# Optimization experiments

Measured on AMD Instinct MI355X. Metric: run time of the kernel, lower is better.

The kernel has to match this reference:

```python
import jax, jax.numpy as jnp
import numpy as np

N_TRIALS, T, INPUT_DIM = 32, 512, 64
N, R, OUTPUT_DIM = 4096, 8, 64
DT = 0.1


def setup_inputs() -> dict:
    key = jax.random.key(0)
    k_inp, k_B, k_W, k_m, k_n = jax.random.split(key, 5)
    inp = jax.random.normal(k_inp, (N_TRIALS, T, INPUT_DIM), dtype=jnp.float32)
    B = jax.random.normal(k_B, (N, INPUT_DIM), dtype=jnp.float32)
    W = jax.random.normal(k_W, (OUTPUT_DIM, N), dtype=jnp.float32) / np.sqrt(N)
    m = jax.random.normal(k_m, (N, R), dtype=jnp.float32)
    n = jax.random.normal(k_n, (N, R), dtype=jnp.float32)
    return {"inp": inp, "B": B, "W": W, "m": m, "n": n}


def reference(inp, B, W, m, n):
    # inp: [b, t, i]; B: [N, i]; W: [o, N]; m, n: [N, r]
    n_trials = inp.shape[0]
    # Precompute input projection for all steps: [t, b, N]
    inp_proj = jnp.einsum('bti,ni->tbn', inp, B)

    def step(x, u):
        # x: [b, N] voltage; u: [b, N] projected input at this step
        # sigmoid(x) @ (m n^T / N)^T == ((sigmoid(x) @ n) @ m^T) / N
        rec = (jax.nn.sigmoid(x) @ n) @ m.T / N
        x_new = (1.0 - DT) * x + DT * (rec + u)
        y = jax.nn.sigmoid(x_new) @ W.T  # [b, o]
        return x_new, (x_new, y)

    x0 = jnp.zeros((n_trials, N), dtype=inp.dtype)
    _, (xs, ys) = jax.lax.scan(step, x0, inp_proj)
    # xs: [t, b, N]; ys: [t, b, o]
    x_seq = jnp.concatenate([x0[None], xs], axis=0).transpose(1, 0, 2)  # [b, t+1, N]
    output_seq = ys.transpose(1, 0, 2)  # [b, t, o]
    return (x_seq, output_seq)
```

## Files before the change

### kernel.cpp

```cpp
#include <hip/hip_runtime.h>

static constexpr int BTRIALS = 32;
static constexpr int TSTEPS  = 512;
static constexpr int IDIM    = 64;
static constexpr int NDIM    = 4096;
static constexpr int RDIM    = 8;
static constexpr int ODIM    = 64;

typedef short v8s __attribute__((ext_vector_type(8)));
typedef float v4f __attribute__((ext_vector_type(4)));

__device__ __forceinline__ float fast_sigmoid(float x) {
    float e = __builtin_amdgcn_exp2f(x * -1.44269504088896340736f);
    return __builtin_amdgcn_rcpf(1.0f + e);
}

__device__ __forceinline__ float2 pk_fma(float2 a, float2 b, float2 c) {
    float2 d;
    asm("v_pk_fma_f32 %0, %1, %2, %3" : "=v"(d) : "v"(a), "v"(b), "v"(c));
    return d;
}

template <int CTRL, int RMASK>
__device__ __forceinline__ float dpp_add(float v) {
    int moved = __builtin_amdgcn_update_dpp(0, __float_as_int(v), CTRL, RMASK, 0xf, true);
    return v + __int_as_float(moved);
}

__device__ __forceinline__ float wave_reduce_to_lane63(float v) {
    v = dpp_add<0x111, 0xf>(v);
    v = dpp_add<0x112, 0xf>(v);
    v = dpp_add<0x114, 0xf>(v);
    v = dpp_add<0x118, 0xf>(v);
    v = dpp_add<0x142, 0xa>(v);
    v = dpp_add<0x143, 0xc>(v);
    return v;
}

__device__ __forceinline__ short f2bf(float f) {
    unsigned u = __float_as_uint(f);
    u += 0x7FFFu + ((u >> 16) & 1u);
    return (short)(u >> 16);
}

__global__ __launch_bounds__(256) void split_conv(const float* __restrict__ src,
                                                  unsigned short* __restrict__ hi,
                                                  unsigned short* __restrict__ lo,
                                                  float scale) {
    const int base = (blockIdx.x * 256 + threadIdx.x) * 8;
    float4 a = *(const float4*)(src + base);
    float4 b = *(const float4*)(src + base + 4);
    float v[8] = {a.x, a.y, a.z, a.w, b.x, b.y, b.z, b.w};
    v8s h, l;
    #pragma unroll
    for (int j = 0; j < 8; ++j) {
        float f  = v[j] * scale;
        short hb = f2bf(f);
        h[j] = hb;
        float fh = __uint_as_float(((unsigned)(unsigned short)hb) << 16);
        l[j] = f2bf(f - fh);
    }
    *(v8s*)(hi + base) = h;
    *(v8s*)(lo + base) = l;
}

__global__ __launch_bounds__(256) void wconv(const float* __restrict__ W,
                                             unsigned short* __restrict__ Wb) {
    const int base = (blockIdx.x * 256 + threadIdx.x) * 8;
    float4 a = *(const float4*)(W + base);
    float4 b = *(const float4*)(W + base + 4);
    v8s o;
    o[0] = f2bf(a.x); o[1] = f2bf(a.y); o[2] = f2bf(a.z); o[3] = f2bf(a.w);
    o[4] = f2bf(b.x); o[5] = f2bf(b.y); o[6] = f2bf(b.z); o[7] = f2bf(b.w);
    *(v8s*)(Wb + base) = o;
}

__global__ __launch_bounds__(256) void pre_gemm_mfma(const unsigned short* __restrict__ Ah,
                                                     const unsigned short* __restrict__ Al,
                                                     const unsigned short* __restrict__ Bh,
                                                     const unsigned short* __restrict__ Bl,
                                                     float* __restrict__ u, int t0) {
    const int tid  = threadIdx.x;
    const int lane = tid & 63;
    const int wv   = tid >> 6;
    const int lm   = lane & 15;
    const int kq   = lane >> 4;

    const int mloc = blockIdx.x * 16 + lm;
    const int b    = mloc & 31;
    const int t    = t0 + (mloc >> 5);
    const size_t arow = (size_t)b * TSTEPS + t;

    const unsigned short* pah = Ah + arow * IDIM + kq * 8;
    const unsigned short* pal = Al + arow * IDIM + kq * 8;
    v8s ah0 = *(const v8s*)(pah);
    v8s ah1 = *(const v8s*)(pah + 32);
    v8s al0 = *(const v8s*)(pal);
    v8s al1 = *(const v8s*)(pal + 32);

    const int n0   = wv * 1024;
    const int urow = blockIdx.x * 16 + kq * 4;

    #pragma unroll 2
    for (int nt = 0; nt < 64; ++nt) {
        const int n = n0 + nt * 16 + lm;
        const unsigned short* pbh = Bh + (size_t)n * IDIM + kq * 8;
        const unsigned short* pbl = Bl + (size_t)n * IDIM + kq * 8;
        v8s bh0 = *(const v8s*)(pbh);
        v8s bh1 = *(const v8s*)(pbh + 32);
        v8s bl0 = *(const v8s*)(pbl);
        v8s bl1 = *(const v8s*)(pbl + 32);
        v4f acc = (v4f){0.f, 0.f, 0.f, 0.f};
        acc = __builtin_amdgcn_mfma_f32_16x16x32_bf16(ah0, bl0, acc, 0, 0, 0);
        acc = __builtin_amdgcn_mfma_f32_16x16x32_bf16(al0, bh0, acc, 0, 0, 0);
        acc = __builtin_amdgcn_mfma_f32_16x16x32_bf16(ah1, bl1, acc, 0, 0, 0);
        acc = __builtin_amdgcn_mfma_f32_16x16x32_bf16(al1, bh1, acc, 0, 0, 0);
        acc = __builtin_amdgcn_mfma_f32_16x16x32_bf16(ah0, bh0, acc, 0, 0, 0);
        acc = __builtin_amdgcn_mfma_f32_16x16x32_bf16(ah1, bh1, acc, 0, 0, 0);
        float* up = u + (size_t)urow * NDIM + n0 + nt * 16 + lm;
        #pragma unroll
        for (int r = 0; r < 4; ++r) up[(size_t)r * NDIM] = acc[r];
    }
}

__global__ __launch_bounds__(512, 2) void scan_kernel(const float* __restrict__ mmat,
                                                      const float* __restrict__ nmat,
                                                      const float* __restrict__ u,
                                                      float* __restrict__ xseq,
                                                      float* __restrict__ xstate,
                                                      unsigned short* __restrict__ sbuf,
                                                      int t0, int tc) {
    const int b    = blockIdx.x;
    const int tid  = threadIdx.x;
    const int j0   = tid * 8;
    const int lane = tid & 63;
    const int wv   = tid >> 6;

    __shared__ __align__(16) float wlds[2][64];

    float2 nmp[4][8], mmp[4][8], x2[4], sp[4];
    const float mscale = 0.1f / 4096.0f;
    #pragma unroll
    for (int jp = 0; jp < 4; ++jp) {
        const float4* na = (const float4*)(nmat + (size_t)(j0 + 2 * jp) * RDIM);
        float4 a0 = na[0], a1 = na[1], b0 = na[2], b1 = na[3];
        nmp[jp][0] = {a0.x, b0.x}; nmp[jp][1] = {a0.y, b0.y};
        nmp[jp][2] = {a0.z, b0.z}; nmp[jp][3] = {a0.w, b0.w};
        nmp[jp][4] = {a1.x, b1.x}; nmp[jp][5] = {a1.y, b1.y};
        nmp[jp][6] = {a1.z, b1.z}; nmp[jp][7] = {a1.w, b1.w};
        const float4* ma = (const float4*)(mmat + (size_t)(j0 + 2 * jp) * RDIM);
        float4 d0 = ma[0], d1 = ma[1], e0 = ma[2], e1 = ma[3];
        mmp[jp][0] = {d0.x * mscale, e0.x * mscale}; mmp[jp][1] = {d0.y * mscale, e0.y * mscale};
        mmp[jp][2] = {d0.z * mscale, e0.z * mscale}; mmp[jp][3] = {d0.w * mscale, e0.w * mscale};
        mmp[jp][4] = {d1.x * mscale, e1.x * mscale}; mmp[jp][5] = {d1.y * mscale, e1.y * mscale};
        mmp[jp][6] = {d1.z * mscale, e1.z * mscale}; mmp[jp][7] = {d1.w * mscale, e1.w * mscale};
    }

    if (t0 == 0) {
        #pragma unroll
        for (int jp = 0; jp < 4; ++jp) x2[jp] = {0.f, 0.f};
        float* z = xseq + (size_t)b * (TSTEPS + 1) * NDIM + j0;
        *(float4*)(z + 0) = make_float4(0.f, 0.f, 0.f, 0.f);
        *(float4*)(z + 4) = make_float4(0.f, 0.f, 0.f, 0.f);
    } else {
        const float* xs = xstate + (size_t)b * NDIM + j0;
        float4 v0 = *(const float4*)(xs + 0);
        float4 v1 = *(const float4*)(xs + 4);
        x2[0] = {v0.x, v0.y}; x2[1] = {v0.z, v0.w};
        x2[2] = {v1.x, v1.y}; x2[3] = {v1.z, v1.w};
    }
    #pragma unroll
    for (int jp = 0; jp < 4; ++jp)
        sp[jp] = {fast_sigmoid(x2[jp].x), fast_sigmoid(x2[jp].y)};

    float2 uvp[4];
    {
        const float* up = u + ((size_t)0 * BTRIALS + b) * NDIM + j0;
        float4 v0 = *(const float4*)(up + 0);
        float4 v1 = *(const float4*)(up + 4);
        uvp[0] = {v0.x, v0.y}; uvp[1] = {v0.z, v0.w};
        uvp[2] = {v1.x, v1.y}; uvp[3] = {v1.z, v1.w};
    }
    const float2 c09 = {0.9f, 0.9f};

    for (int tl = 0; tl < tc; ++tl) {
        const int buf = tl & 1;
        const int tn = (tl + 1 < tc) ? (tl + 1) : tl;
        const float* upn = u + ((size_t)tn * BTRIALS + b) * NDIM + j0;
        float4 pf0 = *(const float4*)(upn + 0);
        float4 pf1 = *(const float4*)(upn + 4);

        float2 p2[8];
        #pragma unroll
        for (int r = 0; r < 8; ++r) p2[r] = {0.f, 0.f};
        #pragma unroll
        for (int jp = 0; jp < 4; ++jp) {
            #pragma unroll
            for (int r = 0; r < 8; ++r) p2[r] = pk_fma(sp[jp], nmp[jp][r], p2[r]);
        }
        float part[8];
        #pragma unroll
        for (int r = 0; r < 8; ++r) part[r] = p2[r].x + p2[r].y;
        #pragma unroll
        for (int r = 0; r < 8; ++r) part[r] = wave_reduce_to_lane63(part[r]);

        if (lane == 63) {
            #pragma unroll
            for (int r = 0; r < 8; ++r) wlds[buf][r * 8 + wv] = part[r];
        }

        float2 xd2[4];
        #pragma unroll
        for (int jp = 0; jp < 4; ++jp) xd2[jp] = pk_fma(c09, x2[jp], uvp[jp]);

        __syncthreads();

        float v = wlds[buf][lane];
        v = dpp_add<0x111, 0xf>(v);
        v = dpp_add<0x112, 0xf>(v);
        v = dpp_add<0x114, 0xf>(v);

        float ps[8];
        #pragma unroll
        for (int r = 0; r < 8; ++r)
            ps[r] = __int_as_float(__builtin_amdgcn_readlane(__float_as_int(v), r * 8 + 7));

        #pragma unroll
        for (int r = 0; r < 8; ++r) {
            float2 psr = {ps[r], ps[r]};
            #pragma unroll
            for (int jp = 0; jp < 4; ++jp) xd2[jp] = pk_fma(psr, mmp[jp][r], xd2[jp]);
        }
        #pragma unroll
        for (int jp = 0; jp < 4; ++jp) x2[jp] = xd2[jp];

        float* xrow = xseq + ((size_t)b * (TSTEPS + 1) + (t0 + tl + 1)) * NDIM + j0;
        *(float4*)(xrow + 0) = make_float4(x2[0].x, x2[0].y, x2[1].x, x2[1].y);
        *(float4*)(xrow + 4) = make_float4(x2[2].x, x2[2].y, x2[3].x, x2[3].y);

        #pragma unroll
        for (int jp = 0; jp < 4; ++jp)
            sp[jp] = {fast_sigmoid(x2[jp].x), fast_sigmoid(x2[jp].y)};
        int c0, c1, c2, c3;
        asm("v_cvt_pk_bf16_f32 %0, %1, %2" : "=v"(c0) : "v"(sp[0].x), "v"(sp[0].y));
        asm("v_cvt_pk_bf16_f32 %0, %1, %2" : "=v"(c1) : "v"(sp[1].x), "v"(sp[1].y));
        asm("v_cvt_pk_bf16_f32 %0, %1, %2" : "=v"(c2) : "v"(sp[2].x), "v"(sp[2].y));
        asm("v_cvt_pk_bf16_f32 %0, %1, %2" : "=v"(c3) : "v"(sp[3].x), "v"(sp[3].y));
        *(int4*)((void*)(sbuf + ((size_t)b * tc + tl) * NDIM + j0)) = make_int4(c0, c1, c2, c3);

        uvp[0] = {pf0.x, pf0.y}; uvp[1] = {pf0.z, pf0.w};
        uvp[2] = {pf1.x, pf1.y}; uvp[3] = {pf1.z, pf1.w};
    }

    float* xs = xstate + (size_t)b * NDIM + j0;
    *(float4*)(xs + 0) = make_float4(x2[0].x, x2[0].y, x2[1].x, x2[1].y);
    *(float4*)(xs + 4) = make_float4(x2[2].x, x2[2].y, x2[3].x, x2[3].y);
}

__global__ __launch_bounds__(256) void y_gemm(const unsigned short* __restrict__ sbuf,
                                              const unsigned short* __restrict__ Wb,
                                              float* __restrict__ yout,
                                              int t0, int tc) {
    const int tid  = threadIdx.x;
    const int lane = tid & 63;
    const int w    = blockIdx.x * 4 + (tid >> 6);
    const int mt   = w >> 1;
    const int ob   = (w & 1) << 1;
    const int lm   = lane & 15;
    const int kq   = lane >> 4;

    const int tilesPerB = tc >> 4;
    const int b  = mt / tilesPerB;
    const int tt = mt % tilesPerB;

    const unsigned short* pa = sbuf + ((size_t)b * tc + tt * 16 + lm) * NDIM + kq * 8;
    const unsigned short* pw0 = Wb + (size_t)(ob * 16 + lm) * NDIM + kq * 8;
    const unsigned short* pw1 = pw0 + (size_t)16 * NDIM;

    v4f acc0 = (v4f){0.f, 0.f, 0.f, 0.f};
    v4f acc1 = (v4f){0.f, 0.f, 0.f, 0.f};

    #pragma unroll 4
    for (int kc = 0; kc < NDIM; kc += 32) {
        v8s af = *(const v8s*)(pa + kc);
        v8s bf0 = *(const v8s*)(pw0 + kc);
        v8s bf1 = *(const v8s*)(pw1 + kc);
        acc0 = __builtin_amdgcn_mfma_f32_16x16x32_bf16(af, bf0, acc0, 0, 0, 0);
        acc1 = __builtin_amdgcn_mfma_f32_16x16x32_bf16(af, bf1, acc1, 0, 0, 0);
    }

    #pragma unroll
    for (int r = 0; r < 4; ++r) {
        const int row = b * TSTEPS + t0 + tt * 16 + kq * 4 + r;
        yout[(size_t)row * ODIM + (ob + 0) * 16 + lm] = acc0[r];
        yout[(size_t)row * ODIM + (ob + 1) * 16 + lm] = acc1[r];
    }
}

extern "C" void kernel_launch(void* const* d_in, const int* in_sizes, int n_in,
                              void* d_out, int out_size, void* d_ws, size_t ws_size,
                              hipStream_t stream) {
    const float* inp = (const float*)d_in[0];
    const float* Bm  = (const float*)d_in[1];
    const float* Wm  = (const float*)d_in[2];
    const float* mm  = (const float*)d_in[3];
    const float* nm  = (const float*)d_in[4];

    float* out  = (float*)d_out;
    float* xseq = out;
    float* yout = out + (size_t)BTRIALS * (TSTEPS + 1) * NDIM;

    float* xstate      = (float*)d_ws;
    unsigned short* Wb = (unsigned short*)(xstate + (size_t)BTRIALS * NDIM);
    unsigned short* Ah = Wb + (size_t)ODIM * NDIM;
    unsigned short* Al = Ah + (size_t)BTRIALS * TSTEPS * IDIM;
    unsigned short* Bh = Al + (size_t)BTRIALS * TSTEPS * IDIM;
    unsigned short* Bl = Bh + (size_t)NDIM * IDIM;
    float* ubuf        = (float*)(Bl + (size_t)NDIM * IDIM);

    const size_t head = (size_t)((char*)ubuf - (char*)d_ws);
    const size_t perstep = (size_t)BTRIALS * NDIM * (sizeof(float) + sizeof(unsigned short));
    size_t avail = (ws_size > head) ? (ws_size - head) : 0;
    int Tc = (int)(avail / perstep);
    if (Tc > TSTEPS) Tc = TSTEPS;
    Tc &= ~15;
    if (Tc < 16) Tc = 16;

    wconv<<<(ODIM * NDIM) / (256 * 8), 256, 0, stream>>>(Wm, Wb);
    split_conv<<<(BTRIALS * TSTEPS * IDIM) / (256 * 8), 256, 0, stream>>>(inp, Ah, Al, 0.1f);
    split_conv<<<(NDIM * IDIM) / (256 * 8), 256, 0, stream>>>(Bm, Bh, Bl, 1.0f);

    for (int t0 = 0; t0 < TSTEPS; t0 += Tc) {
        const int tc = (TSTEPS - t0 < Tc) ? (TSTEPS - t0) : Tc;
        unsigned short* sbuf = (unsigned short*)(ubuf + (size_t)tc * BTRIALS * NDIM);
        const int rows = tc * BTRIALS;
        pre_gemm_mfma<<<rows / 16, 256, 0, stream>>>(Ah, Al, Bh, Bl, ubuf, t0);
        scan_kernel<<<BTRIALS, 512, 0, stream>>>(mm, nm, ubuf, xseq, xstate, sbuf, t0, tc);
        const int mtiles = BTRIALS * (tc / 16);
        y_gemm<<<mtiles / 2, 256, 0, stream>>>(sbuf, Wb, yout, t0, tc);
    }
}
```

Measured before the change: 1.071 ms.

## Fuse pre-GEMM, scan and output GEMM into one persistent flag-synchronised kernel

Replaces the per-chunk sequence of three kernel launches with a single persistent kernel. 32 blocks run the recurrent scan, one per trial, while the remaining 224 blocks act as workers that compute the input projection and the output GEMM. Workers signal chunk completion through atomic flags in workspace, so the scan can start on a chunk as soon as its input projection is ready and the y GEMM can run behind the scan, overlapping the three stages. The scheme depends on all 256 blocks being co-resident and on spin-waits with a timeout break. It also requires a workspace large enough to hold u and sbuf for all 512 timesteps, and the flags share the start of the workspace with the former x-state region.

```diff
diff --git a/kernel.cpp b/kernel.cpp
--- a/kernel.cpp
+++ b/kernel.cpp
@@ -6,6 +6,17 @@
 static constexpr int NDIM    = 4096;
 static constexpr int RDIM    = 8;
 static constexpr int ODIM    = 64;
+
+static constexpr int TC   = 64;
+static constexpr int NCH  = TSTEPS / TC;
+static constexpr int SCAN_BLOCKS  = 32;
+static constexpr int TOTAL_BLOCKS = 256;
+static constexpr int WORKER_WAVES = (TOTAL_BLOCKS - SCAN_BLOCKS) * 8;
+static constexpr int PRE_TASKS_PER_CHUNK = 512;
+static constexpr int PRE_TASKS = NCH * PRE_TASKS_PER_CHUNK;
+static constexpr int Y_TASKS_PER_CHUNK = 256;
+static constexpr int Y_TASKS = NCH * Y_TASKS_PER_CHUNK;
+
 
 typedef short v8s __attribute__((ext_vector_type(8)));
 typedef float v4f __attribute__((ext_vector_type(4)));
@@ -65,7 +76,11 @@
 }
 
 __global__ __launch_bounds__(256) void wconv(const float* __restrict__ W,
-                                             unsigned short* __restrict__ Wb) {
+                                             unsigned short* __restrict__ Wb,
+                                             unsigned* __restrict__ flags) {
+    if (blockIdx.x == 0) {
+        for (int i = threadIdx.x; i < 1024; i += 256) flags[i] = 0;
+    }
     const int base = (blockIdx.x * 256 + threadIdx.x) * 8;
     float4 a = *(const float4*)(W + base);
     float4 b = *(const float4*)(W + base + 4);
@@ -75,225 +90,250 @@
     *(v8s*)(Wb + base) = o;
 }
 
-__global__ __launch_bounds__(256) void pre_gemm_mfma(const unsigned short* __restrict__ Ah,
-                                                     const unsigned short* __restrict__ Al,
-                                                     const unsigned short* __restrict__ Bh,
-                                                     const unsigned short* __restrict__ Bl,
-                                                     float* __restrict__ u, int t0) {
+__global__ __launch_bounds__(512) void mega(const unsigned short* __restrict__ Ah,
+                                            const unsigned short* __restrict__ Al,
+                                            const unsigned short* __restrict__ Bh,
+                                            const unsigned short* __restrict__ Bl,
+                                            const float* __restrict__ mmat,
+                                            const float* __restrict__ nmat,
+                                            float* __restrict__ u,
+                                            float* __restrict__ xseq,
+                                            unsigned short* __restrict__ sbuf,
+                                            const unsigned short* __restrict__ Wb,
+                                            float* __restrict__ yout,
+                                            unsigned* __restrict__ flags) {
+    __shared__ __align__(16) float wlds[2][64];
     const int tid  = threadIdx.x;
     const int lane = tid & 63;
-    const int wv   = tid >> 6;
-    const int lm   = lane & 15;
-    const int kq   = lane >> 4;
-
-    const int mloc = blockIdx.x * 16 + lm;
-    const int b    = mloc & 31;
-    const int t    = t0 + (mloc >> 5);
-    const size_t arow = (size_t)b * TSTEPS + t;
-
-    const unsigned short* pah = Ah + arow * IDIM + kq * 8;
-    const unsigned short* pal = Al + arow * IDIM + kq * 8;
-    v8s ah0 = *(const v8s*)(pah);
-    v8s ah1 = *(const v8s*)(pah + 32);
-    v8s al0 = *(const v8s*)(pal);
-    v8s al1 = *(const v8s*)(pal + 32);
-
-    const int n0   = wv * 1024;
-    const int urow = blockIdx.x * 16 + kq * 4;
-
-    #pragma unroll 2
-    for (int nt = 0; nt < 64; ++nt) {
-        const int n = n0 + nt * 16 + lm;
-        const unsigned short* pbh = Bh + (size_t)n * IDIM + kq * 8;
-        const unsigned short* pbl = Bl + (size_t)n * IDIM + kq * 8;
-        v8s bh0 = *(const v8s*)(pbh);
-        v8s bh1 = *(const v8s*)(pbh + 32);
-        v8s bl0 = *(const v8s*)(pbl);
-        v8s bl1 = *(const v8s*)(pbl + 32);
-        v4f acc = (v4f){0.f, 0.f, 0.f, 0.f};
-        acc = __builtin_amdgcn_mfma_f32_16x16x32_bf16(ah0, bl0, acc, 0, 0, 0);
-        acc = __builtin_amdgcn_mfma_f32_16x16x32_bf16(al0, bh0, acc, 0, 0, 0);
-        acc = __builtin_amdgcn_mfma_f32_16x16x32_bf16(ah1, bl1, acc, 0, 0, 0);
-        acc = __builtin_amdgcn_mfma_f32_16x16x32_bf16(al1, bh1, acc, 0, 0, 0);
-        acc = __builtin_amdgcn_mfma_f32_16x16x32_bf16(ah0, bh0, acc, 0, 0, 0);
-        acc = __builtin_amdgcn_mfma_f32_16x16x32_bf16(ah1, bh1, acc, 0, 0, 0);
-        float* up = u + (size_t)urow * NDIM + n0 + nt * 16 + lm;
+
+    if (blockIdx.x < SCAN_BLOCKS) {
+        const int b  = blockIdx.x;
+        const int j0 = tid * 8;
+        const int wv = tid >> 6;
+
+        float2 nmp[4][8], mmp[4][8], x2[4], sp[4];
+        const float mscale = 0.1f / 4096.0f;
         #pragma unroll
-        for (int r = 0; r < 4; ++r) up[(size_t)r * NDIM] = acc[r];
-    }
-}
-
-__global__ __launch_bounds__(512, 2) void scan_kernel(const float* __restrict__ mmat,
-                                                      const float* __restrict__ nmat,
-                                                      const float* __restrict__ u,
-                                                      float* __restrict__ xseq,
-                                                      float* __restrict__ xstate,
-                                                      unsigned short* __restrict__ sbuf,
-                                                      int t0, int tc) {
-    const int b    = blockIdx.x;
-    const int tid  = threadIdx.x;
-    const int j0   = tid * 8;
-    const int lane = tid & 63;
-    const int wv   = tid >> 6;
-
-    __shared__ __align__(16) float wlds[2][64];
-
-    float2 nmp[4][8], mmp[4][8], x2[4], sp[4];
-    const float mscale = 0.1f / 4096.0f;
-    #pragma unroll
-    for (int jp = 0; jp < 4; ++jp) {
-        const float4* na = (const float4*)(nmat + (size_t)(j0 + 2 * jp) * RDIM);
-        float4 a0 = na[0], a1 = na[1], b0 = na[2], b1 = na[3];
-        nmp[jp][0] = {a0.x, b0.x}; nmp[jp][1] = {a0.y, b0.y};
-        nmp[jp][2] = {a0.z, b0.z}; nmp[jp][3] = {a0.w, b0.w};
-        nmp[jp][4] = {a1.x, b1.x}; nmp[jp][5] = {a1.y, b1.y};
-        nmp[jp][6] = {a1.z, b1.z}; nmp[jp][7] = {a1.w, b1.w};
-        const float4* ma = (const float4*)(mmat + (size_t)(j0 + 2 * jp) * RDIM);
-        float4 d0 = ma[0], d1 = ma[1], e0 = ma[2], e1 = ma[3];
-        mmp[jp][0] = {d0.x * mscale, e0.x * mscale}; mmp[jp][1] = {d0.y * mscale, e0.y * mscale};
-        mmp[jp][2] = {d0.z * mscale, e0.z * mscale}; mmp[jp][3] = {d0.w * mscale, e0.w * mscale};
-        mmp[jp][4] = {d1.x * mscale, e1.x * mscale}; mmp[jp][5] = {d1.y * mscale, e1.y * mscale};
-        mmp[jp][6] = {d1.z * mscale, e1.z * mscale}; mmp[jp][7] = {d1.w * mscale, e1.w * mscale};
-    }
-
-    if (t0 == 0) {
+        for (int jp = 0; jp < 4; ++jp) {
+            const float4* na = (const float4*)(nmat + (size_t)(j0 + 2 * jp) * RDIM);
+            float4 a0 = na[0], a1 = na[1], b0 = na[2], b1 = na[3];
+            nmp[jp][0] = {a0.x, b0.x}; nmp[jp][1] = {a0.y, b0.y};
+            nmp[jp][2] = {a0.z, b0.z}; nmp[jp][3] = {a0.w, b0.w};
+            nmp[jp][4] = {a1.x, b1.x}; nmp[jp][5] = {a1.y, b1.y};
+            nmp[jp][6] = {a1.z, b1.z}; nmp[jp][7] = {a1.w, b1.w};
+            const float4* ma = (const float4*)(mmat + (size_t)(j0 + 2 * jp) * RDIM);
+            float4 d0 = ma[0], d1 = ma[1], e0 = ma[2], e1 = ma[3];
+            mmp[jp][0] = {d0.x * mscale, e0.x * mscale}; mmp[jp][1] = {d0.y * mscale, e0.y * mscale};
+            mmp[jp][2] = {d0.z * mscale, e0.z * mscale}; mmp[jp][3] = {d0.w * mscale, e0.w * mscale};
+            mmp[jp][4] = {d1.x * mscale, e1.x * mscale}; mmp[jp][5] = {d1.y * mscale, e1.y * mscale};
+            mmp[jp][6] = {d1.z * mscale, e1.z * mscale}; mmp[jp][7] = {d1.w * mscale, e1.w * mscale};
+        }
+
         #pragma unroll
         for (int jp = 0; jp < 4; ++jp) x2[jp] = {0.f, 0.f};
-        float* z = xseq + (size_t)b * (TSTEPS + 1) * NDIM + j0;
-        *(float4*)(z + 0) = make_float4(0.f, 0.f, 0.f, 0.f);
-        *(float4*)(z + 4) = make_float4(0.f, 0.f, 0.f, 0.f);
-    } else {
-        const float* xs = xstate + (size_t)b * NDIM + j0;
-        float4 v0 = *(const float4*)(xs + 0);
-        float4 v1 = *(const float4*)(xs + 4);
-        x2[0] = {v0.x, v0.y}; x2[1] = {v0.z, v0.w};
-        x2[2] = {v1.x, v1.y}; x2[3] = {v1.z, v1.w};
-    }
-    #pragma unroll
-    for (int jp = 0; jp < 4; ++jp)
-        sp[jp] = {fast_sigmoid(x2[jp].x), fast_sigmoid(x2[jp].y)};
-
-    float2 uvp[4];
-    {
-        const float* up = u + ((size_t)0 * BTRIALS + b) * NDIM + j0;
-        float4 v0 = *(const float4*)(up + 0);
-        float4 v1 = *(const float4*)(up + 4);
-        uvp[0] = {v0.x, v0.y}; uvp[1] = {v0.z, v0.w};
-        uvp[2] = {v1.x, v1.y}; uvp[3] = {v1.z, v1.w};
-    }
-    const float2 c09 = {0.9f, 0.9f};
-
-    for (int tl = 0; tl < tc; ++tl) {
-        const int buf = tl & 1;
-        const int tn = (tl + 1 < tc) ? (tl + 1) : tl;
-        const float* upn = u + ((size_t)tn * BTRIALS + b) * NDIM + j0;
-        float4 pf0 = *(const float4*)(upn + 0);
-        float4 pf1 = *(const float4*)(upn + 4);
-
-        float2 p2[8];
-        #pragma unroll
-        for (int r = 0; r < 8; ++r) p2[r] = {0.f, 0.f};
-        #pragma unroll
-        for (int jp = 0; jp < 4; ++jp) {
-            #pragma unroll
-            for (int r = 0; r < 8; ++r) p2[r] = pk_fma(sp[jp], nmp[jp][r], p2[r]);
-        }
-        float part[8];
-        #pragma unroll
-        for (int r = 0; r < 8; ++r) part[r] = p2[r].x + p2[r].y;
-        #pragma unroll
-        for (int r = 0; r < 8; ++r) part[r] = wave_reduce_to_lane63(part[r]);
-
-        if (lane == 63) {
-            #pragma unroll
-            for (int r = 0; r < 8; ++r) wlds[buf][r * 8 + wv] = part[r];
-        }
-
-        float2 xd2[4];
-        #pragma unroll
-        for (int jp = 0; jp < 4; ++jp) xd2[jp] = pk_fma(c09, x2[jp], uvp[jp]);
-
-        __syncthreads();
-
-        float v = wlds[buf][lane];
-        v = dpp_add<0x111, 0xf>(v);
-        v = dpp_add<0x112, 0xf>(v);
-        v = dpp_add<0x114, 0xf>(v);
-
-        float ps[8];
-        #pragma unroll
-        for (int r = 0; r < 8; ++r)
-            ps[r] = __int_as_float(__builtin_amdgcn_readlane(__float_as_int(v), r * 8 + 7));
-
-        #pragma unroll
-        for (int r = 0; r < 8; ++r) {
-            float2 psr = {ps[r], ps[r]};
-            #pragma unroll
-            for (int jp = 0; jp < 4; ++jp) xd2[jp] = pk_fma(psr, mmp[jp][r], xd2[jp]);
-        }
-        #pragma unroll
-        for (int jp = 0; jp < 4; ++jp) x2[jp] = xd2[jp];
-
-        float* xrow = xseq + ((size_t)b * (TSTEPS + 1) + (t0 + tl + 1)) * NDIM + j0;
-        *(float4*)(xrow + 0) = make_float4(x2[0].x, x2[0].y, x2[1].x, x2[1].y);
-        *(float4*)(xrow + 4) = make_float4(x2[2].x, x2[2].y, x2[3].x, x2[3].y);
-
+        {
+            float* z = xseq + (size_t)b * (TSTEPS + 1) * NDIM + j0;
+            *(float4*)(z + 0) = make_float4(0.f, 0.f, 0.f, 0.f);
+            *(float4*)(z + 4) = make_float4(0.f, 0.f, 0.f, 0.f);
+        }
         #pragma unroll
         for (int jp = 0; jp < 4; ++jp)
             sp[jp] = {fast_sigmoid(x2[jp].x), fast_sigmoid(x2[jp].y)};
-        int c0, c1, c2, c3;
-        asm("v_cvt_pk_bf16_f32 %0, %1, %2" : "=v"(c0) : "v"(sp[0].x), "v"(sp[0].y));
-        asm("v_cvt_pk_bf16_f32 %0, %1, %2" : "=v"(c1) : "v"(sp[1].x), "v"(sp[1].y));
-        asm("v_cvt_pk_bf16_f32 %0, %1, %2" : "=v"(c2) : "v"(sp[2].x), "v"(sp[2].y));
-        asm("v_cvt_pk_bf16_f32 %0, %1, %2" : "=v"(c3) : "v"(sp[3].x), "v"(sp[3].y));
-        *(int4*)((void*)(sbuf + ((size_t)b * tc + tl) * NDIM + j0)) = make_int4(c0, c1, c2, c3);
-
-        uvp[0] = {pf0.x, pf0.y}; uvp[1] = {pf0.z, pf0.w};
-        uvp[2] = {pf1.x, pf1.y}; uvp[3] = {pf1.z, pf1.w};
-    }
-
-    float* xs = xstate + (size_t)b * NDIM + j0;
-    *(float4*)(xs + 0) = make_float4(x2[0].x, x2[0].y, x2[1].x, x2[1].y);
-    *(float4*)(xs + 4) = make_float4(x2[2].x, x2[2].y, x2[3].x, x2[3].y);
-}
-
-__global__ __launch_bounds__(256) void y_gemm(const unsigned short* __restrict__ sbuf,
-                                              const unsigned short* __restrict__ Wb,
-                                              float* __restrict__ yout,
-                                              int t0, int tc) {
-    const int tid  = threadIdx.x;
-    const int lane = tid & 63;
-    const int w    = blockIdx.x * 4 + (tid >> 6);
-    const int mt   = w >> 1;
-    const int ob   = (w & 1) << 1;
-    const int lm   = lane & 15;
-    const int kq   = lane >> 4;
-
-    const int tilesPerB = tc >> 4;
-    const int b  = mt / tilesPerB;
-    const int tt = mt % tilesPerB;
-
-    const unsigned short* pa = sbuf + ((size_t)b * tc + tt * 16 + lm) * NDIM + kq * 8;
-    const unsigned short* pw0 = Wb + (size_t)(ob * 16 + lm) * NDIM + kq * 8;
-    const unsigned short* pw1 = pw0 + (size_t)16 * NDIM;
-
-    v4f acc0 = (v4f){0.f, 0.f, 0.f, 0.f};
-    v4f acc1 = (v4f){0.f, 0.f, 0.f, 0.f};
-
-    #pragma unroll 4
-    for (int kc = 0; kc < NDIM; kc += 32) {
-        v8s af = *(const v8s*)(pa + kc);
-        v8s bf0 = *(const v8s*)(pw0 + kc);
-        v8s bf1 = *(const v8s*)(pw1 + kc);
-        acc0 = __builtin_amdgcn_mfma_f32_16x16x32_bf16(af, bf0, acc0, 0, 0, 0);
-        acc1 = __builtin_amdgcn_mfma_f32_16x16x32_bf16(af, bf1, acc1, 0, 0, 0);
-    }
-
-    #pragma unroll
-    for (int r = 0; r < 4; ++r) {
-        const int row = b * TSTEPS + t0 + tt * 16 + kq * 4 + r;
-        yout[(size_t)row * ODIM + (ob + 0) * 16 + lm] = acc0[r];
-        yout[(size_t)row * ODIM + (ob + 1) * 16 + lm] = acc1[r];
+
+        const float2 c09 = {0.9f, 0.9f};
+
+        for (int c = 0; c < NCH; ++c) {
+            if (tid == 0) {
+                unsigned spins = 0;
+                while (__hip_atomic_load(&flags[c * 16], __ATOMIC_ACQUIRE,
+                                         __HIP_MEMORY_SCOPE_AGENT) < (unsigned)PRE_TASKS_PER_CHUNK) {
+                    if (++spins > 50000000u) break;
+                }
+            }
+            __syncthreads();
+
+            const int tbase = c * TC;
+            float2 uvp[4];
+            {
+                const float* up = u + ((size_t)tbase * BTRIALS + b) * NDIM + j0;
+                float4 v0 = *(const float4*)(up + 0);
+                float4 v1 = *(const float4*)(up + 4);
+                uvp[0] = {v0.x, v0.y}; uvp[1] = {v0.z, v0.w};
+                uvp[2] = {v1.x, v1.y}; uvp[3] = {v1.z, v1.w};
+            }
+
+            for (int tl = 0; tl < TC; ++tl) {
+                const int t   = tbase + tl;
+                const int buf = tl & 1;
+                const int tn  = tbase + ((tl + 1 < TC) ? tl + 1 : TC - 1);
+                const float* upn = u + ((size_t)tn * BTRIALS + b) * NDIM + j0;
+                float4 pf0 = *(const float4*)(upn + 0);
+                float4 pf1 = *(const float4*)(upn + 4);
+
+                float2 p2[8];
+                #pragma unroll
+                for (int r = 0; r < 8; ++r) p2[r] = {0.f, 0.f};
+                #pragma unroll
+                for (int jp = 0; jp < 4; ++jp) {
+                    #pragma unroll
+                    for (int r = 0; r < 8; ++r) p2[r] = pk_fma(sp[jp], nmp[jp][r], p2[r]);
+                }
+                float part[8];
+                #pragma unroll
+                for (int r = 0; r < 8; ++r) part[r] = p2[r].x + p2[r].y;
+                #pragma unroll
+                for (int r = 0; r < 8; ++r) part[r] = wave_reduce_to_lane63(part[r]);
+
+                if (lane == 63) {
+                    #pragma unroll
+                    for (int r = 0; r < 8; ++r) wlds[buf][r * 8 + wv] = part[r];
+                }
+
+                float2 xd2[4];
+                #pragma unroll
+                for (int jp = 0; jp < 4; ++jp) xd2[jp] = pk_fma(c09, x2[jp], uvp[jp]);
+
+                __syncthreads();
+
+                float v = wlds[buf][lane];
+                v = dpp_add<0x111, 0xf>(v);
+                v = dpp_add<0x112, 0xf>(v);
+                v = dpp_add<0x114, 0xf>(v);
+
+                float ps[8];
+                #pragma unroll
+                for (int r = 0; r < 8; ++r)
+                    ps[r] = __int_as_float(__builtin_amdgcn_readlane(__float_as_int(v), r * 8 + 7));
+
+                #pragma unroll
+                for (int r = 0; r < 8; ++r) {
+                    float2 psr = {ps[r], ps[r]};
+                    #pragma unroll
+                    for (int jp = 0; jp < 4; ++jp) xd2[jp] = pk_fma(psr, mmp[jp][r], xd2[jp]);
+                }
+                #pragma unroll
+                for (int jp = 0; jp < 4; ++jp) x2[jp] = xd2[jp];
+
+                float* xrow = xseq + ((size_t)b * (TSTEPS + 1) + (t + 1)) * NDIM + j0;
+                *(float4*)(xrow + 0) = make_float4(x2[0].x, x2[0].y, x2[1].x, x2[1].y);
+                *(float4*)(xrow + 4) = make_float4(x2[2].x, x2[2].y, x2[3].x, x2[3].y);
+
+                #pragma unroll
+                for (int jp = 0; jp < 4; ++jp)
+                    sp[jp] = {fast_sigmoid(x2[jp].x), fast_sigmoid(x2[jp].y)};
+                int c0, c1, c2, c3;
+                asm("v_cvt_pk_bf16_f32 %0, %1, %2" : "=v"(c0) : "v"(sp[0].x), "v"(sp[0].y));
+                asm("v_cvt_pk_bf16_f32 %0, %1, %2" : "=v"(c1) : "v"(sp[1].x), "v"(sp[1].y));
+                asm("v_cvt_pk_bf16_f32 %0, %1, %2" : "=v"(c2) : "v"(sp[2].x), "v"(sp[2].y));
+                asm("v_cvt_pk_bf16_f32 %0, %1, %2" : "=v"(c3) : "v"(sp[3].x), "v"(sp[3].y));
+                unsigned long long s0 = (unsigned)c0 | ((unsigned long long)(unsigned)c1 << 32);
+                unsigned long long s1 = (unsigned)c2 | ((unsigned long long)(unsigned)c3 << 32);
+                unsigned long long* sp8 =
+                    (unsigned long long*)(sbuf + ((size_t)b * TSTEPS + t) * NDIM + j0);
+                __hip_atomic_store(sp8 + 0, s0, __ATOMIC_RELAXED, __HIP_MEMORY_SCOPE_AGENT);
+                __hip_atomic_store(sp8 + 1, s1, __ATOMIC_RELAXED, __HIP_MEMORY_SCOPE_AGENT);
+
+                uvp[0] = {pf0.x, pf0.y}; uvp[1] = {pf0.z, pf0.w};
+                uvp[2] = {pf1.x, pf1.y}; uvp[3] = {pf1.z, pf1.w};
+            }
+
+            __syncthreads();
+            if (tid == 0)
+                __hip_atomic_store(&flags[128 + b * 16], (unsigned)(c + 1),
+                                   __ATOMIC_RELEASE, __HIP_MEMORY_SCOPE_AGENT);
+        }
+    } else {
+        const int gw = (blockIdx.x - SCAN_BLOCKS) * 8 + (tid >> 6);
+        const int lm = lane & 15;
+        const int kq = lane >> 4;
+
+        for (int T = gw; T < PRE_TASKS; T += WORKER_WAVES) {
+            const int c = T >> 9;
+            const int w = T & 511;
+            const int btile = c * 128 + (w >> 2);
+            const int n0 = (w & 3) * 1024;
+            const int mloc = btile * 16 + lm;
+            const int bb = mloc & 31;
+            const int t  = mloc >> 5;
+            const size_t arow = (size_t)bb * TSTEPS + t;
+
+            const unsigned short* pah = Ah + arow * IDIM + kq * 8;
+            const unsigned short* pal = Al + arow * IDIM + kq * 8;
+            v8s ah0 = *(const v8s*)(pah);
+            v8s ah1 = *(const v8s*)(pah + 32);
+            v8s al0 = *(const v8s*)(pal);
+            v8s al1 = *(const v8s*)(pal + 32);
+
+            const int urow = btile * 16 + kq * 4;
+
+            #pragma unroll 2
+            for (int nt = 0; nt < 64; ++nt) {
+                const int n = n0 + nt * 16 + lm;
+                const unsigned short* pbh = Bh + (size_t)n * IDIM + kq * 8;
+                const unsigned short* pbl = Bl + (size_t)n * IDIM + kq * 8;
+                v8s bh0 = *(const v8s*)(pbh);
+                v8s bh1 = *(const v8s*)(pbh + 32);
+                v8s bl0 = *(const v8s*)(pbl);
+                v8s bl1 = *(const v8s*)(pbl + 32);
+                v4f acc = (v4f){0.f, 0.f, 0.f, 0.f};
+                acc = __builtin_amdgcn_mfma_f32_16x16x32_bf16(ah0, bl0, acc, 0, 0, 0);
+                acc = __builtin_amdgcn_mfma_f32_16x16x32_bf16(al0, bh0, acc, 0, 0, 0);
+                acc = __builtin_amdgcn_mfma_f32_16x16x32_bf16(ah1, bl1, acc, 0, 0, 0);
+                acc = __builtin_amdgcn_mfma_f32_16x16x32_bf16(al1, bh1, acc, 0, 0, 0);
+                acc = __builtin_amdgcn_mfma_f32_16x16x32_bf16(ah0, bh0, acc, 0, 0, 0);
+                acc = __builtin_amdgcn_mfma_f32_16x16x32_bf16(ah1, bh1, acc, 0, 0, 0);
+                float* up = u + (size_t)urow * NDIM + n0 + nt * 16 + lm;
+                #pragma unroll
+                for (int r = 0; r < 4; ++r)
+                    __hip_atomic_store(up + (size_t)r * NDIM, acc[r],
+                                       __ATOMIC_RELAXED, __HIP_MEMORY_SCOPE_AGENT);
+            }
+            if (lane == 0)
+                __hip_atomic_fetch_add(&flags[c * 16], 1u,
+                                       __ATOMIC_RELEASE, __HIP_MEMORY_SCOPE_AGENT);
+        }
+
+        for (int Y = gw; Y < Y_TASKS; Y += WORKER_WAVES) {
+            const int c   = Y >> 8;
+            const int rem = Y & 255;
+            const int bb  = rem >> 3;
+            const int ttl = (rem >> 1) & 3;
+            const int ob  = (rem & 1) << 1;
+            const int ttile = c * 4 + ttl;
+
+            if (lane == 0) {
+                unsigned spins = 0;
+                while (__hip_atomic_load(&flags[128 + bb * 16], __ATOMIC_ACQUIRE,
+                                         __HIP_MEMORY_SCOPE_AGENT) < (unsigned)(c + 1)) {
+                    if (++spins > 50000000u) break;
+                }
+            }
+            asm volatile("" ::: "memory");
+
+            const unsigned short* pa =
+                sbuf + ((size_t)bb * TSTEPS + ttile * 16 + lm) * NDIM + kq * 8;
+            const unsigned short* pw0 = Wb + (size_t)(ob * 16 + lm) * NDIM + kq * 8;
+            const unsigned short* pw1 = pw0 + (size_t)16 * NDIM;
+
+            v4f acc0 = (v4f){0.f, 0.f, 0.f, 0.f};
+            v4f acc1 = (v4f){0.f, 0.f, 0.f, 0.f};
+
+            #pragma unroll 4
+            for (int kc = 0; kc < NDIM; kc += 32) {
+                v8s af  = *(const v8s*)(pa + kc);
+                v8s bf0 = *(const v8s*)(pw0 + kc);
+                v8s bf1 = *(const v8s*)(pw1 + kc);
+                acc0 = __builtin_amdgcn_mfma_f32_16x16x32_bf16(af, bf0, acc0, 0, 0, 0);
+                acc1 = __builtin_amdgcn_mfma_f32_16x16x32_bf16(af, bf1, acc1, 0, 0, 0);
+            }
+
+            #pragma unroll
+            for (int r = 0; r < 4; ++r) {
+                const int row = bb * TSTEPS + ttile * 16 + kq * 4 + r;
+                yout[(size_t)row * ODIM + (ob + 0) * 16 + lm] = acc0[r];
+                yout[(size_t)row * ODIM + (ob + 1) * 16 + lm] = acc1[r];
+            }
+        }
     }
 }
 
@@ -310,33 +350,20 @@
     float* xseq = out;
     float* yout = out + (size_t)BTRIALS * (TSTEPS + 1) * NDIM;
 
-    float* xstate      = (float*)d_ws;
-    unsigned short* Wb = (unsigned short*)(xstate + (size_t)BTRIALS * NDIM);
+    unsigned* flags    = (unsigned*)d_ws;
+    float* xregion     = (float*)d_ws;
+    unsigned short* Wb = (unsigned short*)(xregion + (size_t)BTRIALS * NDIM);
     unsigned short* Ah = Wb + (size_t)ODIM * NDIM;
     unsigned short* Al = Ah + (size_t)BTRIALS * TSTEPS * IDIM;
     unsigned short* Bh = Al + (size_t)BTRIALS * TSTEPS * IDIM;
     unsigned short* Bl = Bh + (size_t)NDIM * IDIM;
     float* ubuf        = (float*)(Bl + (size_t)NDIM * IDIM);
-
-    const size_t head = (size_t)((char*)ubuf - (char*)d_ws);
-    const size_t perstep = (size_t)BTRIALS * NDIM * (sizeof(float) + sizeof(unsigned short));
-    size_t avail = (ws_size > head) ? (ws_size - head) : 0;
-    int Tc = (int)(avail / perstep);
-    if (Tc > TSTEPS) Tc = TSTEPS;
-    Tc &= ~15;
-    if (Tc < 16) Tc = 16;
-
-    wconv<<<(ODIM * NDIM) / (256 * 8), 256, 0, stream>>>(Wm, Wb);
+    unsigned short* sbuf = (unsigned short*)(ubuf + (size_t)TSTEPS * BTRIALS * NDIM);
+
+    wconv<<<(ODIM * NDIM) / (256 * 8), 256, 0, stream>>>(Wm, Wb, flags);
     split_conv<<<(BTRIALS * TSTEPS * IDIM) / (256 * 8), 256, 0, stream>>>(inp, Ah, Al, 0.1f);
     split_conv<<<(NDIM * IDIM) / (256 * 8), 256, 0, stream>>>(Bm, Bh, Bl, 1.0f);
 
-    for (int t0 = 0; t0 < TSTEPS; t0 += Tc) {
-        const int tc = (TSTEPS - t0 < Tc) ? (TSTEPS - t0) : Tc;
-        unsigned short* sbuf = (unsigned short*)(ubuf + (size_t)tc * BTRIALS * NDIM);
-        const int rows = tc * BTRIALS;
-        pre_gemm_mfma<<<rows / 16, 256, 0, stream>>>(Ah, Al, Bh, Bl, ubuf, t0);
-        scan_kernel<<<BTRIALS, 512, 0, stream>>>(mm, nm, ubuf, xseq, xstate, sbuf, t0, tc);
-        const int mtiles = BTRIALS * (tc / 16);
-        y_gemm<<<mtiles / 2, 256, 0, stream>>>(sbuf, Wb, yout, t0, tc);
-    }
-}
+    mega<<<TOTAL_BLOCKS, 512, 0, stream>>>(Ah, Al, Bh, Bl, mm, nm,
+                                           ubuf, xseq, sbuf, Wb, yout, flags);
+}
```

Measured after the change: 2.453 ms. 2.29x slower.
